# Performance work log

Measured on AMD Instinct MI355X. Metric: run time of the kernel, lower is better.

## Reference

```python
import jax, jax.numpy as jnp
import numpy as np

ITERATIONS = 3


def setup_inputs() -> dict:
    key = jax.random.key(0)
    ks = jax.random.split(key, 12)
    B, S, H = 16, 128, 256
    N_LABELS, N_SLOTS = 22, 122
    sc = 0.02
    return {
        "h": jax.random.normal(ks[0], (B, S, H), jnp.float32),
        "c_slot": jax.random.normal(ks[1], (B, S, H), jnp.float32),
        "c_inte": jax.random.normal(ks[2], (B, H), jnp.float32),
        # weights stored as [in, out]; applied as x @ W (equivalent to torch Linear on random init)
        "W_SF": jax.random.normal(ks[3], (H, H), jnp.float32) * sc,
        "V_SF": jax.random.normal(ks[4], (H, H), jnp.float32) * sc,
        "V1_ID": jax.random.normal(ks[5], (H, H), jnp.float32) * sc,
        "V2_ID_w": jax.random.normal(ks[6], (H, H), jnp.float32) * sc,
        "V2_ID_b": jax.random.normal(ks[7], (H,), jnp.float32) * sc,
        "w_ID": jax.random.normal(ks[8], (H,), jnp.float32) * sc,
        "W_inte_ans": jax.random.normal(ks[9], (2 * H, N_LABELS), jnp.float32) * sc,
        "W_slot_ans": jax.random.normal(ks[10], (2 * H, N_SLOTS), jnp.float32) * sc,
    }


def reference(h, c_slot, c_inte, W_SF, V_SF, V1_ID, V2_ID_w, V2_ID_b, w_ID,
              W_inte_ans, W_slot_ans):
    B, S, H = h.shape
    diag = jnp.arange(S)
    r_inte = c_inte
    r_slot = c_slot  # placeholder; always overwritten in first iteration
    for _ in range(ITERATIONS):
        # SF step
        f = jnp.tanh(c_slot + (r_inte @ W_SF)[:, None, :])        # [B,S,H]
        f = (f @ V_SF).sum(axis=1)                                # [B,H]
        r_slot = f[:, None, :] * c_slot                           # [B,S,H]
        # ID step: pairwise additive attention, diagonal of row-softmax
        sf = r_slot @ V1_ID                                       # [B,S,H]
        hf = h @ V2_ID_w + V2_ID_b                                # [B,S,H]
        # scores[b,i,j] = w_ID . tanh(sf[b,i] + hf[b,j])
        scores = jnp.einsum('bijh,h->bij',
                            jnp.tanh(sf[:, :, None, :] + hf[:, None, :, :]),
                            w_ID)                                 # [B,S,S]
        probs = jax.nn.softmax(scores, axis=-1)                   # softmax over j
        alphas = probs[:, diag, diag]                             # [B,S]
        r = (r_slot * alphas[:, :, None]).sum(axis=1)             # [B,H]
        r_inte = r + c_inte
    intent_output = jnp.concatenate([r_inte, h[:, S - 1, :]], axis=-1) @ W_inte_ans
    slot_output = jnp.concatenate([h, r_slot], axis=-1) @ W_slot_ans
    return slot_output, intent_output
```

## Files before the change

### kernel.cpp

```cpp
#include <hip/hip_runtime.h>

#define Bn 16
#define Sn 128
#define Hn 256
#define NLn 22
#define NSn 122

#define K2c 2.8853900817779268f
#define L2Ec 1.4426950408889634f

__device__ __forceinline__ float fexp2(float x) { return __builtin_amdgcn_exp2f(x); }
__device__ __forceinline__ float frcp(float x) { return __builtin_amdgcn_rcpf(x); }

union F4 { float4 v; float f[4]; };

__device__ __forceinline__ void A_body(const float* __restrict__ c_slot,
                                       const float* __restrict__ c_inte,
                                       const float* __restrict__ W_SF,
                                       const float* __restrict__ V_SF,
                                       const float* __restrict__ alphas,
                                       float* __restrict__ g2,
                                       int b, int use_alpha,
                                       float* rL, float* fLq, float* aL,
                                       float (*pt)[Hn]) {
  const int tid = threadIdx.x;
  const int h = tid & (Hn - 1);
  const int kq = tid >> 8;

  if (use_alpha) {
    if (tid < Sn) aL[tid] = alphas[b * Sn + tid];
    __syncthreads();
    float ps = 0.f;
    #pragma unroll 8
    for (int s = kq * 32; s < kq * 32 + 32; ++s)
      ps += c_slot[(size_t)(b * Sn + s) * Hn + h] * aL[s];
    pt[kq][h] = ps;
    __syncthreads();
    if (!kq)
      rL[h] = c_inte[b * Hn + h] +
              g2[b * Hn + h] * (pt[0][h] + pt[1][h] + pt[2][h] + pt[3][h]);
  } else {
    if (!kq) rL[h] = c_inte[b * Hn + h];
  }
  __syncthreads();

  float pm = 0.f;
  #pragma unroll 8
  for (int k = kq * 64; k < kq * 64 + 64; ++k)
    pm += rL[k] * W_SF[(size_t)k * Hn + h];
  __syncthreads();
  pt[kq][h] = pm;
  __syncthreads();
  const float m = pt[0][h] + pt[1][h] + pt[2][h] + pt[3][h];
  const float em = fexp2(fminf(fmaxf(K2c * m, -60.f), 60.f));

  float pr = 0.f;
  #pragma unroll 8
  for (int s = kq * 32; s < kq * 32 + 32; ++s) {
    float zc = fminf(fmaxf(K2c * c_slot[(size_t)(b * Sn + s) * Hn + h], -60.f), 60.f);
    pr += frcp(fmaf(fexp2(zc), em, 1.f));
  }
  __syncthreads();
  pt[kq][h] = pr;
  __syncthreads();
  if (!kq) fLq[h] = (float)Sn - 2.f * (pt[0][h] + pt[1][h] + pt[2][h] + pt[3][h]);
  __syncthreads();

  float pg = 0.f;
  #pragma unroll 8
  for (int k = kq * 64; k < kq * 64 + 64; ++k)
    pg += fLq[k] * V_SF[(size_t)k * Hn + h];
  __syncthreads();
  pt[kq][h] = pg;
  __syncthreads();
  if (!kq)
    g2[b * Hn + h] = pt[0][h] + pt[1][h] + pt[2][h] + pt[3][h];
}

__global__ __launch_bounds__(1024) void k_hfA(const float* __restrict__ hp,
                                              const float* __restrict__ V2w,
                                              const float* __restrict__ V2b,
                                              const float* __restrict__ c_slot,
                                              const float* __restrict__ c_inte,
                                              const float* __restrict__ W_SF,
                                              const float* __restrict__ V_SF,
                                              float* __restrict__ ZT,
                                              float* __restrict__ g2) {
  __shared__ float xT[Hn][8];
  __shared__ float pp[3][Hn][8];
  __shared__ float rL[Hn];
  __shared__ float fLq[Hn];
  __shared__ float aL[Sn];
  __shared__ float pt[4][Hn];
  const int tid = threadIdx.x;
  const int blk = blockIdx.x;

  if (blk >= 256) {
    A_body(c_slot, c_inte, W_SF, V_SF, nullptr, g2, blk - 256, 0,
           rL, fLq, aL, pt);
    return;
  }

  const int r0 = blk * 8;
  const int b = r0 >> 7;
  const int j0 = r0 & (Sn - 1);
  const int h = tid & (Hn - 1);
  const int kh = tid >> 8;
  xT[h][kh * 2]     = hp[(size_t)(r0 + kh * 2) * Hn + h];
  xT[h][kh * 2 + 1] = hp[(size_t)(r0 + kh * 2 + 1) * Hn + h];
  __syncthreads();
  float acc[8] = {0.f, 0.f, 0.f, 0.f, 0.f, 0.f, 0.f, 0.f};
  #pragma unroll 8
  for (int k = kh * 64; k < kh * 64 + 64; ++k) {
    const float v = V2w[(size_t)k * Hn + h];
    F4 xa, xb;
    xa.v = *(const float4*)&xT[k][0];
    xb.v = *(const float4*)&xT[k][4];
    acc[0] += xa.f[0] * v; acc[1] += xa.f[1] * v;
    acc[2] += xa.f[2] * v; acc[3] += xa.f[3] * v;
    acc[4] += xb.f[0] * v; acc[5] += xb.f[1] * v;
    acc[6] += xb.f[2] * v; acc[7] += xb.f[3] * v;
  }
  if (kh) {
    F4 s0, s1;
    s0.f[0] = acc[0]; s0.f[1] = acc[1]; s0.f[2] = acc[2]; s0.f[3] = acc[3];
    s1.f[0] = acc[4]; s1.f[1] = acc[5]; s1.f[2] = acc[6]; s1.f[3] = acc[7];
    *(float4*)&pp[kh - 1][h][0] = s0.v;
    *(float4*)&pp[kh - 1][h][4] = s1.v;
  }
  __syncthreads();
  if (!kh) {
    const float bj = V2b[h];
    F4 o0, o1;
    #pragma unroll
    for (int i = 0; i < 8; ++i) {
      float z = K2c * (acc[i] + pp[0][h][i] + pp[1][h][i] + pp[2][h][i] + bj);
      z = fminf(fmaxf(z, -60.f), 60.f);
      if (i < 4) o0.f[i] = fexp2(z); else o1.f[i - 4] = fexp2(z);
    }
    *(float4*)&ZT[((size_t)b * Hn + h) * Sn + j0] = o0.v;
    *(float4*)&ZT[((size_t)b * Hn + h) * Sn + j0 + 4] = o1.v;
  }
}

__global__ __launch_bounds__(1024) void k_A(const float* __restrict__ c_slot,
                                            const float* __restrict__ c_inte,
                                            const float* __restrict__ W_SF,
                                            const float* __restrict__ V_SF,
                                            const float* __restrict__ alphas,
                                            float* __restrict__ g2) {
  __shared__ float rL[Hn];
  __shared__ float fLq[Hn];
  __shared__ float aL[Sn];
  __shared__ float pt[4][Hn];
  A_body(c_slot, c_inte, W_SF, V_SF, alphas, g2, blockIdx.x, 1,
         rL, fLq, aL, pt);
}

__global__ __launch_bounds__(1024) void k_C(const float* __restrict__ c_slot,
                                            const float* __restrict__ V1,
                                            const float* __restrict__ g2,
                                            const float* __restrict__ ZT,
                                            const float* __restrict__ wid,
                                            float* __restrict__ alphas,
                                            const float* __restrict__ hp,
                                            const float* __restrict__ Ws,
                                            float* __restrict__ outS) {
  __shared__ union Shm {
    struct {
      float bufA[Hn][4];
      float bufB[Hn][4];
      union { float pp[3][Hn][4]; float red[7][4][Sn]; } u;
      float sc4[4][Sn];
      float wL[Hn];
    } c;
    struct {
      float bufA[Hn][8];
      float bufB[Hn][8];
      float red[7][8][Sn];
    } s;
  } shm;

  const int tid = threadIdx.x;
  const int blk = blockIdx.x;

  if (blk >= 512) {
    const int sb = blk - 512;
    const int r0 = sb * 8;
    const int b2 = r0 >> 7;
    const int h = tid & (Hn - 1);
    const int q4 = tid >> 8;
    const float gv = g2[b2 * Hn + h];
    #pragma unroll
    for (int i = 0; i < 2; ++i) {
      const int row = q4 * 2 + i;
      shm.s.bufA[h][row] = hp[(size_t)(r0 + row) * Hn + h];
      shm.s.bufB[h][row] = gv * c_slot[(size_t)(r0 + row) * Hn + h];
    }
    __syncthreads();
    const int jc = tid & 127;
    const int k8 = tid >> 7;
    float acc[8] = {0.f, 0.f, 0.f, 0.f, 0.f, 0.f, 0.f, 0.f};
    if (jc < NSn) {
      const float (*xb)[8] = (k8 < 4) ? shm.s.bufA : shm.s.bufB;
      const int kg0 = k8 * 64;
      const int koff = (k8 < 4) ? 0 : 256;
      #pragma unroll 8
      for (int u = 0; u < 64; ++u) {
        const float v = Ws[(size_t)(kg0 + u) * NSn + jc];
        F4 xa, xb4;
        xa.v = *(const float4*)&xb[kg0 - koff + u][0];
        xb4.v = *(const float4*)&xb[kg0 - koff + u][4];
        acc[0] += xa.f[0] * v; acc[1] += xa.f[1] * v;
        acc[2] += xa.f[2] * v; acc[3] += xa.f[3] * v;
        acc[4] += xb4.f[0] * v; acc[5] += xb4.f[1] * v;
        acc[6] += xb4.f[2] * v; acc[7] += xb4.f[3] * v;
      }
    }
    if (k8) {
      #pragma unroll
      for (int i = 0; i < 8; ++i) shm.s.red[k8 - 1][i][jc] = acc[i];
    }
    __syncthreads();
    if (!k8 && jc < NSn) {
      #pragma unroll
      for (int i = 0; i < 8; ++i) {
        float tot = acc[i];
        #pragma unroll
        for (int r = 0; r < 7; ++r) tot += shm.s.red[r][i][jc];
        outS[(size_t)(r0 + i) * NSn + jc] = tot;
      }
    }
    return;
  }

  const int b = blk >> 5;
  const int i0 = (blk & 31) * 4;
  const int h = tid & (Hn - 1);
  const int kq = tid >> 8;

  shm.c.bufA[h][kq] = g2[b * Hn + h] * c_slot[(size_t)(b * Sn + i0 + kq) * Hn + h];
  if (tid < Hn) shm.c.wL[tid] = wid[tid];
  __syncthreads();

  {
    float acc[4] = {0.f, 0.f, 0.f, 0.f};
    #pragma unroll 8
    for (int k = kq * 64; k < kq * 64 + 64; ++k) {
      const float v = V1[(size_t)k * Hn + h];
      F4 xa; xa.v = *(const float4*)&shm.c.bufA[k][0];
      acc[0] += xa.f[0] * v; acc[1] += xa.f[1] * v;
      acc[2] += xa.f[2] * v; acc[3] += xa.f[3] * v;
    }
    if (kq) {
      F4 s0;
      s0.f[0] = acc[0]; s0.f[1] = acc[1]; s0.f[2] = acc[2]; s0.f[3] = acc[3];
      *(float4*)&shm.c.u.pp[kq - 1][h][0] = s0.v;
    }
    __syncthreads();
    if (!kq) {
      #pragma unroll
      for (int i = 0; i < 4; ++i) {
        float z = K2c * (acc[i] + shm.c.u.pp[0][h][i] + shm.c.u.pp[1][h][i] +
                         shm.c.u.pp[2][h][i]);
        z = fminf(fmaxf(z, -60.f), 60.f);
        shm.c.bufB[h][i] = fexp2(z);
      }
    }
  }
  __syncthreads();

  const int j = tid & (Sn - 1);
  const int hq = tid >> 7;
  float a4[4] = {0.f, 0.f, 0.f, 0.f};
  const float* zp = ZT + ((size_t)b * Hn + hq * 32) * Sn + j;
  #pragma unroll 4
  for (int hh = 0; hh < 32; ++hh) {
    const float z = zp[(size_t)hh * Sn];
    const float wh = shm.c.wL[hq * 32 + hh];
    F4 ya; ya.v = *(const float4*)&shm.c.bufB[hq * 32 + hh][0];
    a4[0] += wh * frcp(fmaf(ya.f[0], z, 1.f));
    a4[1] += wh * frcp(fmaf(ya.f[1], z, 1.f));
    a4[2] += wh * frcp(fmaf(ya.f[2], z, 1.f));
    a4[3] += wh * frcp(fmaf(ya.f[3], z, 1.f));
  }
  if (hq) {
    #pragma unroll
    for (int i = 0; i < 4; ++i) shm.c.u.red[hq - 1][i][j] = a4[i];
  }
  __syncthreads();
  if (!hq) {
    #pragma unroll
    for (int i = 0; i < 4; ++i) {
      float tot = a4[i];
      #pragma unroll
      for (int r = 0; r < 7; ++r) tot += shm.c.u.red[r][i][j];
      shm.c.sc4[i][j] = -2.f * L2Ec * tot;
    }
  }
  __syncthreads();

  if (tid < 128) {
    const int row = tid >> 5;
    const int l5 = tid & 31;
    const float v0 = shm.c.sc4[row][l5];
    const float v1 = shm.c.sc4[row][l5 + 32];
    const float v2 = shm.c.sc4[row][l5 + 64];
    const float v3 = shm.c.sc4[row][l5 + 96];
    float mx = fmaxf(fmaxf(v0, v1), fmaxf(v2, v3));
    #pragma unroll
    for (int o = 16; o >= 1; o >>= 1) mx = fmaxf(mx, __shfl_xor(mx, o, 32));
    float sm = fexp2(v0 - mx) + fexp2(v1 - mx) + fexp2(v2 - mx) + fexp2(v3 - mx);
    #pragma unroll
    for (int o = 16; o >= 1; o >>= 1) sm += __shfl_xor(sm, o, 32);
    if (l5 == 0) {
      const int ig = i0 + row;
      alphas[b * Sn + ig] = fexp2(shm.c.sc4[row][ig] - mx) * frcp(sm);
    }
  }
}

__global__ __launch_bounds__(512) void k_int(const float* __restrict__ hp,
                                             const float* __restrict__ c_slot,
                                             const float* __restrict__ c_inte,
                                             const float* __restrict__ g2,
                                             const float* __restrict__ alphas,
                                             const float* __restrict__ Wi,
                                             float* __restrict__ outI) {
  __shared__ float aL[Sn];
  __shared__ float cv[2 * Hn];
  __shared__ float ptA[2][Hn];
  __shared__ float ip[NLn][16];
  const int b = blockIdx.x;
  const int tid = threadIdx.x;
  if (tid < Sn) aL[tid] = alphas[b * Sn + tid];
  __syncthreads();
  const int h = tid & (Hn - 1);
  const int k2 = tid >> 8;
  float ps = 0.f;
  #pragma unroll 8
  for (int s = k2 * 64; s < k2 * 64 + 64; ++s)
    ps += c_slot[(size_t)(b * Sn + s) * Hn + h] * aL[s];
  ptA[k2][h] = ps;
  __syncthreads();
  if (!k2) {
    cv[h] = c_inte[b * Hn + h] + g2[b * Hn + h] * (ptA[0][h] + ptA[1][h]);
    cv[Hn + h] = hp[(size_t)(b * Sn + Sn - 1) * Hn + h];
  }
  __syncthreads();
  if (tid < NLn * 16) {
    const int l = tid >> 4, c = tid & 15;
    float p = 0.f;
    #pragma unroll
    for (int k = c * 32; k < c * 32 + 32; ++k) p += cv[k] * Wi[k * NLn + l];
    ip[l][c] = p;
  }
  __syncthreads();
  if (tid < NLn) {
    float t = 0.f;
    #pragma unroll
    for (int c = 0; c < 16; ++c) t += ip[tid][c];
    outI[b * NLn + tid] = t;
  }
}

extern "C" void kernel_launch(void* const* d_in, const int* in_sizes, int n_in,
                              void* d_out, int out_size, void* d_ws, size_t ws_size,
                              hipStream_t stream) {
  const float* hp     = (const float*)d_in[0];
  const float* c_slot = (const float*)d_in[1];
  const float* c_inte = (const float*)d_in[2];
  const float* W_SF   = (const float*)d_in[3];
  const float* V_SF   = (const float*)d_in[4];
  const float* V1     = (const float*)d_in[5];
  const float* V2w    = (const float*)d_in[6];
  const float* V2b    = (const float*)d_in[7];
  const float* wid    = (const float*)d_in[8];
  const float* Wi     = (const float*)d_in[9];
  const float* Ws     = (const float*)d_in[10];
  float* outS = (float*)d_out;
  float* outI = (float*)d_out + Bn * Sn * NSn;

  float* ws = (float*)d_ws;
  float* ZT     = ws;
  float* g2     = ZT + (size_t)Bn * Sn * Hn;
  float* alphas = g2 + Bn * Hn;

  hipLaunchKernelGGL(k_hfA, dim3(256 + Bn), dim3(1024), 0, stream,
                     hp, V2w, V2b, c_slot, c_inte, W_SF, V_SF, ZT, g2);
  hipLaunchKernelGGL(k_C, dim3(512), dim3(1024), 0, stream,
                     c_slot, V1, g2, ZT, wid, alphas, hp, Ws, outS);
  for (int it = 1; it < 3; ++it) {
    hipLaunchKernelGGL(k_A, dim3(Bn), dim3(1024), 0, stream,
                       c_slot, c_inte, W_SF, V_SF, alphas, g2);
    hipLaunchKernelGGL(k_C, dim3(it == 2 ? 768 : 512), dim3(1024), 0, stream,
                       c_slot, V1, g2, ZT, wid, alphas, hp, Ws, outS);
  }
  hipLaunchKernelGGL(k_int, dim3(Bn), dim3(512), 0, stream,
                     hp, c_slot, c_inte, g2, alphas, Wi, outI);
}
```

Baseline: 107.8 us.

## Process eight query rows per k_C block and pair tanh reciprocals

Each attention block of k_C now handles 8 query rows instead of 4, halving the number of attention blocks from 512 to 256. Each ZT and V1 load is reused across twice as many rows. The score loop combines two h-terms per reciprocal, computing (w1*B + w2*A)/(A*B), which halves rcp instructions at the cost of extra multiplies and some overflow risk when the products are large. Block indexing is also reordered so that batch varies fastest. The trade-off is fewer blocks (256 on a 256-CU part), more registers and more shared memory per block.

```diff
diff --git a/kernel.cpp b/kernel.cpp
--- a/kernel.cpp
+++ b/kernel.cpp
@@ -168,10 +168,10 @@
                                             float* __restrict__ outS) {
   __shared__ union Shm {
     struct {
-      float bufA[Hn][4];
-      float bufB[Hn][4];
-      union { float pp[3][Hn][4]; float red[7][4][Sn]; } u;
-      float sc4[4][Sn];
+      float bufA[Hn][8];
+      float bufB[Hn][8];
+      union { float pp[3][Hn][8]; float red[7][8][Sn]; } u;
+      float sc8[8][Sn];
       float wL[Hn];
     } c;
     struct {
@@ -184,8 +184,8 @@
   const int tid = threadIdx.x;
   const int blk = blockIdx.x;
 
-  if (blk >= 512) {
-    const int sb = blk - 512;
+  if (blk >= 256) {
+    const int sb = blk - 256;
     const int r0 = sb * 8;
     const int b2 = r0 >> 7;
     const int h = tid & (Hn - 1);
@@ -234,33 +234,44 @@
     return;
   }
 
-  const int b = blk >> 5;
-  const int i0 = (blk & 31) * 4;
+  const int b = blk & 15;
+  const int i0 = (blk >> 4) * 8;
   const int h = tid & (Hn - 1);
   const int kq = tid >> 8;
 
-  shm.c.bufA[h][kq] = g2[b * Hn + h] * c_slot[(size_t)(b * Sn + i0 + kq) * Hn + h];
-  if (tid < Hn) shm.c.wL[tid] = wid[tid];
-  __syncthreads();
-
   {
-    float acc[4] = {0.f, 0.f, 0.f, 0.f};
+    const float gv = g2[b * Hn + h];
+    const int ii = kq * 2;
+    shm.c.bufA[h][ii]     = gv * c_slot[(size_t)(b * Sn + i0 + ii) * Hn + h];
+    shm.c.bufA[h][ii + 1] = gv * c_slot[(size_t)(b * Sn + i0 + ii + 1) * Hn + h];
+    if (tid < Hn) shm.c.wL[tid] = wid[tid];
+  }
+  __syncthreads();
+
+  {
+    float acc[8] = {0.f, 0.f, 0.f, 0.f, 0.f, 0.f, 0.f, 0.f};
     #pragma unroll 8
     for (int k = kq * 64; k < kq * 64 + 64; ++k) {
       const float v = V1[(size_t)k * Hn + h];
-      F4 xa; xa.v = *(const float4*)&shm.c.bufA[k][0];
+      F4 xa, xb;
+      xa.v = *(const float4*)&shm.c.bufA[k][0];
+      xb.v = *(const float4*)&shm.c.bufA[k][4];
       acc[0] += xa.f[0] * v; acc[1] += xa.f[1] * v;
       acc[2] += xa.f[2] * v; acc[3] += xa.f[3] * v;
+      acc[4] += xb.f[0] * v; acc[5] += xb.f[1] * v;
+      acc[6] += xb.f[2] * v; acc[7] += xb.f[3] * v;
     }
     if (kq) {
-      F4 s0;
+      F4 s0, s1;
       s0.f[0] = acc[0]; s0.f[1] = acc[1]; s0.f[2] = acc[2]; s0.f[3] = acc[3];
+      s1.f[0] = acc[4]; s1.f[1] = acc[5]; s1.f[2] = acc[6]; s1.f[3] = acc[7];
       *(float4*)&shm.c.u.pp[kq - 1][h][0] = s0.v;
+      *(float4*)&shm.c.u.pp[kq - 1][h][4] = s1.v;
     }
     __syncthreads();
     if (!kq) {
       #pragma unroll
-      for (int i = 0; i < 4; ++i) {
+      for (int i = 0; i < 8; ++i) {
         float z = K2c * (acc[i] + shm.c.u.pp[0][h][i] + shm.c.u.pp[1][h][i] +
                          shm.c.u.pp[2][h][i]);
         z = fminf(fmaxf(z, -60.f), 60.f);
@@ -272,41 +283,58 @@
 
   const int j = tid & (Sn - 1);
   const int hq = tid >> 7;
-  float a4[4] = {0.f, 0.f, 0.f, 0.f};
+  float a8[8] = {0.f, 0.f, 0.f, 0.f, 0.f, 0.f, 0.f, 0.f};
   const float* zp = ZT + ((size_t)b * Hn + hq * 32) * Sn + j;
-  #pragma unroll 4
-  for (int hh = 0; hh < 32; ++hh) {
-    const float z = zp[(size_t)hh * Sn];
-    const float wh = shm.c.wL[hq * 32 + hh];
-    F4 ya; ya.v = *(const float4*)&shm.c.bufB[hq * 32 + hh][0];
-    a4[0] += wh * frcp(fmaf(ya.f[0], z, 1.f));
-    a4[1] += wh * frcp(fmaf(ya.f[1], z, 1.f));
-    a4[2] += wh * frcp(fmaf(ya.f[2], z, 1.f));
-    a4[3] += wh * frcp(fmaf(ya.f[3], z, 1.f));
+  #pragma unroll 2
+  for (int hh = 0; hh < 32; hh += 2) {
+    const float z1 = zp[(size_t)hh * Sn];
+    const float z2 = zp[(size_t)(hh + 1) * Sn];
+    const float w1 = shm.c.wL[hq * 32 + hh];
+    const float w2 = shm.c.wL[hq * 32 + hh + 1];
+    F4 ya1, yb1, ya2, yb2;
+    ya1.v = *(const float4*)&shm.c.bufB[hq * 32 + hh][0];
+    yb1.v = *(const float4*)&shm.c.bufB[hq * 32 + hh][4];
+    ya2.v = *(const float4*)&shm.c.bufB[hq * 32 + hh + 1][0];
+    yb2.v = *(const float4*)&shm.c.bufB[hq * 32 + hh + 1][4];
+    #pragma unroll
+    for (int i = 0; i < 4; ++i) {
+      {
+        const float A = fmaf(ya1.f[i], z1, 1.f);
+        const float B = fmaf(ya2.f[i], z2, 1.f);
+        const float N = fmaf(w1, B, w2 * A);
+        a8[i] = fmaf(N, frcp(A * B), a8[i]);
+      }
+      {
+        const float A = fmaf(yb1.f[i], z1, 1.f);
+        const float B = fmaf(yb2.f[i], z2, 1.f);
+        const float N = fmaf(w1, B, w2 * A);
+        a8[4 + i] = fmaf(N, frcp(A * B), a8[4 + i]);
+      }
+    }
   }
   if (hq) {
     #pragma unroll
-    for (int i = 0; i < 4; ++i) shm.c.u.red[hq - 1][i][j] = a4[i];
+    for (int i = 0; i < 8; ++i) shm.c.u.red[hq - 1][i][j] = a8[i];
   }
   __syncthreads();
   if (!hq) {
     #pragma unroll
-    for (int i = 0; i < 4; ++i) {
-      float tot = a4[i];
+    for (int i = 0; i < 8; ++i) {
+      float tot = a8[i];
       #pragma unroll
       for (int r = 0; r < 7; ++r) tot += shm.c.u.red[r][i][j];
-      shm.c.sc4[i][j] = -2.f * L2Ec * tot;
-    }
-  }
-  __syncthreads();
-
-  if (tid < 128) {
+      shm.c.sc8[i][j] = -2.f * L2Ec * tot;
+    }
+  }
+  __syncthreads();
+
+  if (tid < 256) {
     const int row = tid >> 5;
     const int l5 = tid & 31;
-    const float v0 = shm.c.sc4[row][l5];
-    const float v1 = shm.c.sc4[row][l5 + 32];
-    const float v2 = shm.c.sc4[row][l5 + 64];
-    const float v3 = shm.c.sc4[row][l5 + 96];
+    const float v0 = shm.c.sc8[row][l5];
+    const float v1 = shm.c.sc8[row][l5 + 32];
+    const float v2 = shm.c.sc8[row][l5 + 64];
+    const float v3 = shm.c.sc8[row][l5 + 96];
     float mx = fmaxf(fmaxf(v0, v1), fmaxf(v2, v3));
     #pragma unroll
     for (int o = 16; o >= 1; o >>= 1) mx = fmaxf(mx, __shfl_xor(mx, o, 32));
@@ -315,7 +343,7 @@
     for (int o = 16; o >= 1; o >>= 1) sm += __shfl_xor(sm, o, 32);
     if (l5 == 0) {
       const int ig = i0 + row;
-      alphas[b * Sn + ig] = fexp2(shm.c.sc4[row][ig] - mx) * frcp(sm);
+      alphas[b * Sn + ig] = fexp2(shm.c.sc8[row][ig] - mx) * frcp(sm);
     }
   }
 }
@@ -388,12 +416,10 @@
 
   hipLaunchKernelGGL(k_hfA, dim3(256 + Bn), dim3(1024), 0, stream,
                      hp, V2w, V2b, c_slot, c_inte, W_SF, V_SF, ZT, g2);
-  hipLaunchKernelGGL(k_C, dim3(512), dim3(1024), 0, stream,
-                     c_slot, V1, g2, ZT, wid, alphas, hp, Ws, outS);
-  for (int it = 1; it < 3; ++it) {
-    hipLaunchKernelGGL(k_A, dim3(Bn), dim3(1024), 0, stream,
-                       c_slot, c_inte, W_SF, V_SF, alphas, g2);
-    hipLaunchKernelGGL(k_C, dim3(it == 2 ? 768 : 512), dim3(1024), 0, stream,
+  for (int it = 0; it < 3; ++it) {
+    if (it) hipLaunchKernelGGL(k_A, dim3(Bn), dim3(1024), 0, stream,
+                               c_slot, c_inte, W_SF, V_SF, alphas, g2);
+    hipLaunchKernelGGL(k_C, dim3(it == 2 ? 512 : 256), dim3(1024), 0, stream,
                        c_slot, V1, g2, ZT, wid, alphas, hp, Ws, outS);
   }
   hipLaunchKernelGGL(k_int, dim3(Bn), dim3(512), 0, stream,
```

Result: faster. 103.1 us (-4.3%).
